# Performance work log

Measured on AMD Instinct MI355X. Metric: run time of the kernel, lower is better.

Reference implementation:

```python
import jax, jax.numpy as jnp
import numpy as np

T, IN, OUT, M, C = 8192, 1024, 1024, 128, 32
MIN_PERIOD, MAX_PERIOD = 1.0, 1024.0
LN_EPS = 1e-5


def _linear_params(key, in_f, out_f):
    # equinox nn.Linear default init: U(-1/sqrt(in), 1/sqrt(in)) for weight and bias
    lim = 1.0 / np.sqrt(in_f)
    kw, kb = jax.random.split(key)
    w = jax.random.uniform(kw, (out_f, in_f), minval=-lim, maxval=lim, dtype=jnp.float32)
    b = jax.random.uniform(kb, (out_f,), minval=-lim, maxval=lim, dtype=jnp.float32)
    return w, b


def setup_inputs() -> dict:
    key = jax.random.key(0)
    ks = jax.random.split(key, 8)
    x = jax.random.normal(ks[0], (T, IN), dtype=jnp.float32)
    done = jax.random.bernoulli(ks[1], 0.01, (T,))  # sparse episode resets
    state_re = jnp.zeros((1, M, C), jnp.float32)
    state_im = jnp.zeros((1, M, C), jnp.float32)
    # ffa.init(memory_size, context_size): decay rates a and context frequencies b
    a = jnp.linspace(1e-6, 0.5, M, dtype=jnp.float32)
    b = 2.0 * jnp.pi / jnp.linspace(MIN_PERIOD, MAX_PERIOD, C, dtype=jnp.float32)
    pre_w, pre_b = _linear_params(ks[2], IN, M)
    gin_w, gin_b = _linear_params(ks[3], IN, M)
    gout_w, gout_b = _linear_params(ks[4], IN, OUT)
    skip_w, skip_b = _linear_params(ks[5], IN, OUT)
    mix_w, mix_b = _linear_params(ks[6], 2 * M * C, OUT)
    return dict(x=x, done=done, state_re=state_re, state_im=state_im, a=a, b=b,
                pre_w=pre_w, pre_b=pre_b, gin_w=gin_w, gin_b=gin_b,
                gout_w=gout_w, gout_b=gout_b, skip_w=skip_w, skip_b=skip_b,
                mix_w=mix_w, mix_b=mix_b)


def _ffm_forward(x, done, s0, a, b, pre_w, pre_b, gin_w, gin_b,
                 gout_w, gout_b, skip_w, skip_b, mix_w, mix_b):
    # input gating: gated_x[t, m]
    gate_in = jax.nn.sigmoid(x @ gin_w.T + gin_b)            # [T, M]
    gated_x = (x @ pre_w.T + pre_b) * gate_in                # [T, M]

    # gamma[m, c] = exp(-|a_m| + i b_c): per-step complex decay/rotation
    re, im = jnp.broadcast_arrays(-jnp.abs(a)[:, None], b[None, :])
    gamma = jnp.exp(jax.lax.complex(re, im))                 # [M, C] complex64

    def step(s, inp):
        # s_t = gamma * s_{t-1} * (1 - done_t) + x_t 1^T  (reset before accumulate)
        xt, dt = inp
        keep = jnp.where(dt, 0.0, 1.0).astype(jnp.float32)
        s = keep * s * gamma + xt[:, None]
        return s, s

    _, states = jax.lax.scan(step, s0, (gated_x.astype(jnp.complex64), done))  # [T, M, C]

    # mix: concat(real, imag) along last axis -> [T, M, 2C] -> [T, 2MC]
    z_in = jnp.concatenate([states.real, states.imag], axis=-1).reshape(states.shape[0], -1)
    z = z_in @ mix_w.T + mix_b                               # [T, OUT]

    gate_out = jax.nn.sigmoid(x @ gout_w.T + gout_b)         # [T, OUT]
    skip = x @ skip_w.T + skip_b                             # [T, OUT]

    # LayerNorm without weight/bias (eps = 1e-5)
    zg = z * gate_out
    mu = zg.mean(-1, keepdims=True)
    var = ((zg - mu) ** 2).mean(-1, keepdims=True)
    ln = (zg - mu) / jnp.sqrt(var + LN_EPS)

    out = ln + skip * (1.0 - gate_out)
    return out, states


def reference(x, done, state_re, state_im, a, b, pre_w, pre_b, gin_w, gin_b,
              gout_w, gout_b, skip_w, skip_b, mix_w, mix_b):
    s0 = jax.lax.complex(state_re, state_im)[0]              # [M, C]
    return _ffm_forward(x, done, s0, a, b, pre_w, pre_b, gin_w, gin_b,
                        gout_w, gout_b, skip_w, skip_b, mix_w, mix_b)
```

## Files before the change

kernel.cpp:

```cpp
#include <hip/hip_runtime.h>
#include <stdint.h>

#define T_DIM 8192
#define IN_DIM 1024
#define OUT_DIM 1024
#define M_DIM 128
#define SEG 64
#define NSEG (T_DIM / SEG)
#define CHUNK 2048
#define KS_FB 4

typedef __bf16 bf16x8 __attribute__((ext_vector_type(8)));
typedef float f32x4 __attribute__((ext_vector_type(4)));

__device__ inline unsigned short f2bf(float f) {
  unsigned int u = __float_as_uint(f);
  unsigned int r = (u + 0x7fffu + ((u >> 16) & 1u)) >> 16;
  return (unsigned short)r;
}
__device__ inline float bf2f(unsigned short h) {
  return __uint_as_float(((unsigned int)h) << 16);
}
__device__ inline float sigm(float v) { return 1.f / (1.f + expf(-v)); }

__global__ __launch_bounds__(256) void f2bf_kernel(const float* __restrict__ in,
                                                   unsigned short* __restrict__ out, long n) {
  long i = (long)blockIdx.x * 256 + threadIdx.x;
  if (i < n) out[i] = f2bf(in[i]);
}

__global__ __launch_bounds__(256) void permconv_kernel(const float* __restrict__ w,
                                                       unsigned short* __restrict__ o, long n) {
  long i = (long)blockIdx.x * 256 + threadIdx.x;
  if (i >= n) return;
  long row = i >> 13;
  int k = (int)(i & 8191);
  int src = ((k >> 6) << 6) | ((k & 1) << 5) | ((k >> 1) & 31);
  o[i] = f2bf(w[(row << 13) + src]);
}

__global__ __launch_bounds__(256) void wcat_kernel(const float* __restrict__ gout_w,
                                                   const float* __restrict__ skip_w,
                                                   const float* __restrict__ pre_w,
                                                   const float* __restrict__ gin_w,
                                                   unsigned short* __restrict__ o) {
  long i = (long)blockIdx.x * 256 + threadIdx.x;
  if (i >= (long)2304 * 1024) return;
  int row = (int)(i >> 10), col = (int)(i & 1023);
  float v;
  if (row < 1024)       v = gout_w[row * 1024 + col];
  else if (row < 2048)  v = skip_w[(row - 1024) * 1024 + col];
  else if (row < 2176)  v = pre_w[(row - 2048) * 1024 + col];
  else                  v = gin_w[(row - 2176) * 1024 + col];
  o[i] = f2bf(v);
}

__global__ void bcat_kernel(const float* __restrict__ gout_b, const float* __restrict__ skip_b,
                            const float* __restrict__ pre_b, const float* __restrict__ gin_b,
                            float* __restrict__ dst) {
  int i = blockIdx.x * 256 + threadIdx.x;
  if (i >= 2304) return;
  float v;
  if (i < 1024)      v = gout_b[i];
  else if (i < 2048) v = skip_b[i - 1024];
  else if (i < 2176) v = pre_b[i - 2048];
  else               v = gin_b[i - 2176];
  dst[i] = v;
}

__global__ void gamma_kernel(const float* __restrict__ a, const float* __restrict__ b,
                             float2* __restrict__ gam, float2* __restrict__ gamL) {
  int tid = blockIdx.x * 256 + threadIdx.x;
  int m = tid >> 5, c = tid & 31;
  double aa = fabs((double)a[m]);
  double ang = (double)b[c];
  double mag = exp(-aa);
  gam[tid] = make_float2((float)(mag * cos(ang)), (float)(mag * sin(ang)));
  double magL = exp(-aa * (double)SEG);
  double angL = ang * (double)SEG;
  gamL[tid] = make_float2((float)(magL * cos(angL)), (float)(magL * sin(angL)));
}

#define GEMM_KLOOP(AP, BP, LDK)                                                        \
  for (int k0 = 0; k0 < kloop_end; k0 += 64) {                                         \
    _Pragma("unroll")                                                                  \
    for (int cc = 0; cc < 4; ++cc) {                                                   \
      __builtin_amdgcn_global_load_lds(                                                \
          (const __attribute__((address_space(1))) void*)(AP + k0 + (size_t)cc * 32 * (LDK)), \
          (__attribute__((address_space(3))) void*)(As + cc * 2048 + w * 512), 16, 0, 0);     \
      __builtin_amdgcn_global_load_lds(                                                \
          (const __attribute__((address_space(1))) void*)(BP + k0 + (size_t)cc * 32 * (LDK)), \
          (__attribute__((address_space(3))) void*)(Bs + cc * 2048 + w * 512), 16, 0, 0);     \
    }                                                                                  \
    __syncthreads();                                                                   \
    _Pragma("unroll")                                                                  \
    for (int kk = 0; kk < 2; ++kk) {                                                   \
      const int eb = kk ? e1 : e0;                                                     \
      const char* Bp = (const char*)Bpbase + eb;                                       \
      bf16x8 b0 = *(const bf16x8*)(Bp);                                                \
      bf16x8 b1 = *(const bf16x8*)(Bp + 2048);                                         \
      bf16x8 b2 = *(const bf16x8*)(Bp + 4096);                                         \
      bf16x8 b3 = *(const bf16x8*)(Bp + 6144);                                         \
      const char* Ap = (const char*)Apbase + eb;                                       \
      _Pragma("unroll")                                                                \
      for (int i = 0; i < 4; ++i) {                                                    \
        bf16x8 af = *(const bf16x8*)(Ap + i * 2048);                                   \
        acc[i][0] = __builtin_amdgcn_mfma_f32_16x16x32_bf16(af, b0, acc[i][0], 0, 0, 0);\
        acc[i][1] = __builtin_amdgcn_mfma_f32_16x16x32_bf16(af, b1, acc[i][1], 0, 0, 0);\
        acc[i][2] = __builtin_amdgcn_mfma_f32_16x16x32_bf16(af, b2, acc[i][2], 0, 0, 0);\
        acc[i][3] = __builtin_amdgcn_mfma_f32_16x16x32_bf16(af, b3, acc[i][3], 0, 0, 0);\
      }                                                                                \
    }                                                                                  \
    __syncthreads();                                                                   \
  }

#define GEMM_PREAMBLE                                                                  \
  const int tid = threadIdx.x;                                                         \
  const int lane = tid & 63, w = tid >> 6;                                             \
  const int wr = w >> 1, wc = w & 1;                                                   \
  f32x4 acc[4][4] = {};                                                                \
  const int srow = tid >> 3;                                                           \
  const int ksw = ((tid & 7) ^ (srow & 7)) * 8;                                        \
  const int l15 = lane & 15;                                                           \
  const int krd = (lane >> 4) * 8;                                                     \
  const int rsw = (lane & 7) << 3;                                                     \
  const int e0 = (krd ^ rsw) * 2;                                                      \
  const int e1 = ((32 + krd) ^ rsw) * 2;                                               \
  const unsigned short* Apbase = &As[(wr * 64 + l15) * 64];                            \
  const unsigned short* Bpbase = &Bs[(wc * 64 + l15) * 64];

__global__ __launch_bounds__(256, 4) void gemm_gs_kernel(
    const unsigned short* __restrict__ A, const unsigned short* __restrict__ B,
    const float* __restrict__ bias, unsigned short* __restrict__ gs,
    float* __restrict__ tmp) {
  __shared__ __align__(16) unsigned short As[128 * 64];
  __shared__ __align__(16) unsigned short Bs[128 * 64];
  const int xcd = blockIdx.x & 7;
  const int idx = blockIdx.x >> 3;
  const int bn = idx % 18;
  const int bm = xcd * 8 + idx / 18;
  const int n0 = bn * 128, t0 = bm * 128;
  GEMM_PREAMBLE
  const unsigned short* Ab = A + (size_t)(t0 + srow) * 1024 + ksw;
  const unsigned short* Bb = B + (size_t)(n0 + srow) * 1024 + ksw;
  const int kloop_end = 1024;
  GEMM_KLOOP(Ab, Bb, 1024)

  const int rbase = t0 + wr * 64 + ((lane >> 4) * 4);
  const int cbase = n0 + wc * 64 + l15;
#pragma unroll
  for (int j = 0; j < 4; ++j) {
    const int col = cbase + j * 16;
    const float bv = bias[col];
#pragma unroll
    for (int i = 0; i < 4; ++i) {
#pragma unroll
      for (int r = 0; r < 4; ++r) {
        float v = acc[i][j][r] + bv;
        int row = rbase + i * 16 + r;
        if (col < 2048) gs[(size_t)row * 2048 + col] = f2bf(v);
        else            tmp[(size_t)row * 256 + (col - 2048)] = v;
      }
    }
  }
}

__global__ __launch_bounds__(256, 4) void gemm_splitk_kernel(
    const unsigned short* __restrict__ A, const unsigned short* __restrict__ B,
    float* __restrict__ partials, int nbm, int kslice, int prows, int xcd_map) {
  __shared__ __align__(16) unsigned short As[128 * 64];
  __shared__ __align__(16) unsigned short Bs[128 * 64];
  int bm, bn, ks;
  if (xcd_map) {
    const int xcd = blockIdx.x & 7;
    const int idx = blockIdx.x >> 3;
    ks = xcd >> 2;
    bm = (xcd & 3) * 16 + (idx >> 3);
    bn = idx & 7;
  } else {
    const int cpx = gridDim.x >> 3;
    const int wid = (blockIdx.x & 7) * cpx + (blockIdx.x >> 3);
    bm = wid % nbm;
    bn = (wid / nbm) & 7;
    ks = wid / (nbm * 8);
  }
  const int n0 = bn * 128, t0 = bm * 128;
  GEMM_PREAMBLE
  const unsigned short* Ab = A + (size_t)(t0 + srow) * 8192 + ks * kslice + ksw;
  const unsigned short* Bb = B + (size_t)(n0 + srow) * 8192 + ks * kslice + ksw;
  const int kloop_end = kslice;
  GEMM_KLOOP(Ab, Bb, 8192)

  float* Cp = partials + (size_t)ks * prows * 1024;
  const int rbase = t0 + wr * 64 + ((lane >> 4) * 4);
  const int cbase = n0 + wc * 64 + l15;
#pragma unroll
  for (int j = 0; j < 4; ++j) {
    const int col = cbase + j * 16;
#pragma unroll
    for (int i = 0; i < 4; ++i)
#pragma unroll
      for (int r = 0; r < 4; ++r)
        Cp[(size_t)(rbase + i * 16 + r) * 1024 + col] = acc[i][j][r];
  }
}

__global__ __launch_bounds__(256) void reduce_kernel(const f32x4* __restrict__ partials,
                                                     const f32x4* __restrict__ bias4,
                                                     f32x4* __restrict__ outc) {
  int i = blockIdx.x * 256 + threadIdx.x;
  const size_t stride = (size_t)CHUNK * 256;
  f32x4 s = partials[i];
#pragma unroll
  for (int p = 1; p < KS_FB; ++p) s += partials[(size_t)p * stride + i];
  s += bias4[i & 255];
  outc[i] = s;
}

__global__ __launch_bounds__(256) void gated_kernel(const float* __restrict__ tmp,
                                                    float* __restrict__ gated) {
  int i = blockIdx.x * 256 + threadIdx.x;
  int t = i >> 7, m = i & 127;
  float p = tmp[t * 256 + m];
  float g = tmp[t * 256 + 128 + m];
  gated[i] = p * sigm(g);
}

__global__ __launch_bounds__(256) void scan_p1_kernel(
    const float* __restrict__ gated, const int* __restrict__ done,
    const float2* __restrict__ gam, const float2* __restrict__ gamL,
    float2* __restrict__ carryA, float2* __restrict__ carryB) {
  int gid = blockIdx.x * 256 + threadIdx.x;
  int seg = gid >> 12, tid = gid & 4095;
  int m = tid >> 5;
  float2 g = gam[tid];
  int t0 = seg * SEG;
  float sr = 0.f, si = 0.f, keep_all = 1.f;
  for (int tt = 0; tt < SEG; ++tt) {
    int t = t0 + tt;
    float xv = gated[t * M_DIM + m];
    bool d = done[t] != 0;
    float pr = d ? 0.f : sr;
    float pi = d ? 0.f : si;
    if (d) keep_all = 0.f;
    sr = fmaf(g.x, pr, fmaf(-g.y, pi, xv));
    si = fmaf(g.y, pr, g.x * pi);
  }
  carryB[(size_t)seg * 4096 + tid] = make_float2(sr, si);
  float2 gL = gamL[tid];
  carryA[(size_t)seg * 4096 + tid] = make_float2(keep_all * gL.x, keep_all * gL.y);
}

__global__ __launch_bounds__(256) void scan_p2_kernel(
    const float2* __restrict__ carryA, float2* __restrict__ carryB,
    const float* __restrict__ s0_re, const float* __restrict__ s0_im) {
  int tid = blockIdx.x * 256 + threadIdx.x;
  float sr = s0_re[tid], si = s0_im[tid];
  for (int p = 0; p < NSEG; ++p) {
    size_t idx = (size_t)p * 4096 + tid;
    float2 A = carryA[idx];
    float2 B = carryB[idx];
    carryB[idx] = make_float2(sr, si);
    float nr = fmaf(A.x, sr, fmaf(-A.y, si, B.x));
    float ni = fmaf(A.y, sr, fmaf(A.x, si, B.y));
    sr = nr; si = ni;
  }
}

__global__ __launch_bounds__(256) void scan_p3_kernel(
    const float* __restrict__ gated, const int* __restrict__ done,
    const float2* __restrict__ gam, const float2* __restrict__ segstart,
    float* __restrict__ out_states, int pair_mode,
    unsigned int* __restrict__ st_bf, int tbase) {
  int gid = blockIdx.x * 256 + threadIdx.x;
  int segl = gid >> 12, tid = gid & 4095;
  int m = tid >> 5;
  int seg = tbase / SEG + segl;
  float2 g = gam[tid];
  float2 s = segstart[(size_t)seg * 4096 + tid];
  float sr = s.x, si = s.y;
  int t0 = seg * SEG;
  for (int tt = 0; tt < SEG; ++tt) {
    int t = t0 + tt;
    float xv = gated[t * M_DIM + m];
    bool d = done[t] != 0;
    float pr = d ? 0.f : sr;
    float pi = d ? 0.f : si;
    sr = fmaf(g.x, pr, fmaf(-g.y, pi, xv));
    si = fmaf(g.y, pr, g.x * pi);
    if (pair_mode) {
      ((float2*)out_states)[(size_t)t * 4096 + tid] = make_float2(sr, si);
    } else {
      out_states[(size_t)t * 4096 + tid] = sr;
    }
    st_bf[(size_t)(t - tbase) * 4096 + tid] =
        (unsigned int)f2bf(sr) | ((unsigned int)f2bf(si) << 16);
  }
}

__global__ __launch_bounds__(256) void ln_kernel(const float* __restrict__ partials, int nred,
                                                 const float* __restrict__ mixb,
                                                 const unsigned short* __restrict__ gs,
                                                 float* __restrict__ out) {
  const int t = blockIdx.x;
  const int tid = threadIdx.x;
  __shared__ float sm[8];
  const int o = tid * 4;
  f32x4 z;
  if (nred == 0) {
    z = *(const f32x4*)&out[(size_t)t * 1024 + o];
  } else {
    z = *(const f32x4*)&partials[(size_t)t * 1024 + o];
    for (int p = 1; p < nred; ++p)
      z += *(const f32x4*)&partials[(size_t)p * T_DIM * 1024 + (size_t)t * 1024 + o];
    z += *(const f32x4*)&mixb[o];
  }
  ushort4 gu = *(const ushort4*)&gs[(size_t)t * 2048 + o];
  ushort4 su = *(const ushort4*)&gs[(size_t)t * 2048 + 1024 + o];
  float g[4], sk[4], zg[4];
  g[0] = sigm(bf2f(gu.x)); g[1] = sigm(bf2f(gu.y));
  g[2] = sigm(bf2f(gu.z)); g[3] = sigm(bf2f(gu.w));
  sk[0] = bf2f(su.x); sk[1] = bf2f(su.y); sk[2] = bf2f(su.z); sk[3] = bf2f(su.w);
  float sum = 0.f;
#pragma unroll
  for (int j = 0; j < 4; ++j) { zg[j] = z[j] * g[j]; sum += zg[j]; }
#pragma unroll
  for (int off = 32; off > 0; off >>= 1) sum += __shfl_down(sum, off, 64);
  if ((tid & 63) == 0) sm[tid >> 6] = sum;
  __syncthreads();
  const float mu = (sm[0] + sm[1] + sm[2] + sm[3]) * (1.f / 1024.f);
  float sq = 0.f;
#pragma unroll
  for (int j = 0; j < 4; ++j) { float d = zg[j] - mu; sq += d * d; }
#pragma unroll
  for (int off = 32; off > 0; off >>= 1) sq += __shfl_down(sq, off, 64);
  if ((tid & 63) == 0) sm[4 + (tid >> 6)] = sq;
  __syncthreads();
  const float var = (sm[4] + sm[5] + sm[6] + sm[7]) * (1.f / 1024.f);
  const float rstd = 1.f / sqrtf(var + 1e-5f);
  f32x4 res;
#pragma unroll
  for (int j = 0; j < 4; ++j) res[j] = (zg[j] - mu) * rstd + sk[j] * (1.f - g[j]);
  *(f32x4*)&out[(size_t)t * 1024 + o] = res;
}

extern "C" void kernel_launch(void* const* d_in, const int* in_sizes, int n_in,
                              void* d_out, int out_size, void* d_ws, size_t ws_size,
                              hipStream_t stream) {
  const float* x      = (const float*)d_in[0];
  const int*   done   = (const int*)d_in[1];
  const float* s0_re  = (const float*)d_in[2];
  const float* s0_im  = (const float*)d_in[3];
  const float* a      = (const float*)d_in[4];
  const float* b      = (const float*)d_in[5];
  const float* pre_w  = (const float*)d_in[6];
  const float* pre_b  = (const float*)d_in[7];
  const float* gin_w  = (const float*)d_in[8];
  const float* gin_b  = (const float*)d_in[9];
  const float* gout_w = (const float*)d_in[10];
  const float* gout_b = (const float*)d_in[11];
  const float* skip_w = (const float*)d_in[12];
  const float* skip_b = (const float*)d_in[13];
  const float* mix_w  = (const float*)d_in[14];
  const float* mix_b  = (const float*)d_in[15];

  float* out_f = (float*)d_out;
  float* states_f = out_f + (size_t)T_DIM * OUT_DIM;
  const int pair_mode = (out_size >= 75000000) ? 1 : 0;

  char* ws = (char*)d_ws;
  size_t off = 0;
  auto alloc = [&](size_t bytes) {
    void* p = ws + off;
    off = (off + bytes + 255) & ~(size_t)255;
    return p;
  };
  unsigned short* x_bf   = (unsigned short*)alloc((size_t)T_DIM * IN_DIM * 2);
  unsigned short* Bmix   = (unsigned short*)alloc((size_t)OUT_DIM * 8192 * 2);
  unsigned short* Wgs    = (unsigned short*)alloc((size_t)2304 * IN_DIM * 2);
  float* bias_gs         = (float*)alloc(2304 * 4);
  float* tmp_pg          = (float*)alloc((size_t)T_DIM * 256 * 4);
  float* gated           = (float*)alloc((size_t)T_DIM * M_DIM * 4);
  float2* gam            = (float2*)alloc(4096 * 8);
  float2* gamL           = (float2*)alloc(4096 * 8);
  float2* carryA         = (float2*)alloc((size_t)NSEG * 4096 * 8);
  float2* carryB         = (float2*)alloc((size_t)NSEG * 4096 * 8);
  unsigned short* gs_o   = (unsigned short*)alloc((size_t)T_DIM * 2048 * 2);

  size_t need_main = off + (size_t)T_DIM * 8192 * 2 + (size_t)2 * T_DIM * 1024 * 4 + 1024;
  const int full_path = (ws_size == 0 || ws_size >= need_main) ? 1 : 0;

  dim3 blk(256);
  long nx = (long)T_DIM * IN_DIM;
  f2bf_kernel<<<(unsigned)((nx + 255) / 256), blk, 0, stream>>>(x, x_bf, nx);
  permconv_kernel<<<32768, blk, 0, stream>>>(mix_w, Bmix, 8388608L);
  wcat_kernel<<<9216, blk, 0, stream>>>(gout_w, skip_w, pre_w, gin_w, Wgs);
  bcat_kernel<<<9, blk, 0, stream>>>(gout_b, skip_b, pre_b, gin_b, bias_gs);
  gamma_kernel<<<16, blk, 0, stream>>>(a, b, gam, gamL);

  gemm_gs_kernel<<<1152, blk, 0, stream>>>(x_bf, Wgs, bias_gs, gs_o, tmp_pg);
  gated_kernel<<<(T_DIM * M_DIM) / 256, blk, 0, stream>>>(tmp_pg, gated);

  scan_p1_kernel<<<NSEG * 16, blk, 0, stream>>>(gated, done, gam, gamL, carryA, carryB);
  scan_p2_kernel<<<16, blk, 0, stream>>>(carryA, carryB, s0_re, s0_im);

  if (full_path) {
    unsigned short* st_bf = (unsigned short*)alloc((size_t)T_DIM * 8192 * 2);
    float* partials       = (float*)alloc((size_t)2 * T_DIM * 1024 * 4);
    scan_p3_kernel<<<NSEG * 16, blk, 0, stream>>>(gated, done, gam, carryB,
                                                  states_f, pair_mode,
                                                  (unsigned int*)st_bf, 0);
    gemm_splitk_kernel<<<1024, blk, 0, stream>>>(st_bf, Bmix, partials,
                                                 64, 4096, T_DIM, 1);
    ln_kernel<<<T_DIM, blk, 0, stream>>>(partials, 2, mix_b, gs_o, out_f);
  } else {
    unsigned short* st_bf = (unsigned short*)alloc((size_t)CHUNK * 8192 * 2);
    float* partials       = (float*)alloc((size_t)KS_FB * CHUNK * 1024 * 4);
    for (int ch = 0; ch < T_DIM / CHUNK; ++ch) {
      int tbase = ch * CHUNK;
      scan_p3_kernel<<<(CHUNK / SEG) * 16, blk, 0, stream>>>(gated, done, gam, carryB,
                                                             states_f, pair_mode,
                                                             (unsigned int*)st_bf, tbase);
      gemm_splitk_kernel<<<8 * (CHUNK / 128) * KS_FB, blk, 0, stream>>>(
          st_bf, Bmix, partials, CHUNK / 128, 8192 / KS_FB, CHUNK, 0);
      reduce_kernel<<<CHUNK, blk, 0, stream>>>((const f32x4*)partials, (const f32x4*)mix_b,
                                               (f32x4*)(out_f + (size_t)tbase * OUT_DIM));
    }
    ln_kernel<<<T_DIM, blk, 0, stream>>>(nullptr, 0, mix_b, gs_o, out_f);
  }
  (void)n_in; (void)in_sizes;
}
```

Before: 370.4 us.

## Use 256x256-tile double-buffered GEMM for the mix projection

```diff
diff --git a/kernel.cpp b/kernel.cpp
--- a/kernel.cpp
+++ b/kernel.cpp
@@ -165,25 +165,113 @@
   }
 }
 
+__global__ __launch_bounds__(512, 2) void gemm_mix256_kernel(
+    const unsigned short* __restrict__ A, const unsigned short* __restrict__ B,
+    float* __restrict__ partials) {
+  __shared__ __align__(16) unsigned short As[2][256 * 64];
+  __shared__ __align__(16) unsigned short Bs[2][256 * 64];
+  const int xcd = blockIdx.x & 7;
+  const int idx = blockIdx.x >> 3;
+  const int ks = xcd >> 2;
+  const int bm = (xcd & 3) * 8 + (idx >> 2);
+  const int bn = idx & 3;
+  const int t0 = bm * 256, n0 = bn * 256;
+  const int tid = threadIdx.x;
+  const int lane = tid & 63;
+  const int w8 = tid >> 6;
+  const int wr = w8 >> 2;
+  const int wcol = w8 & 3;
+
+  f32x4 acc[8][4] = {};
+
+  const int srow = tid >> 3;
+  const int ksw = ((tid & 7) ^ (srow & 7)) * 8;
+  const unsigned short* Ab = A + (size_t)(t0 + srow) * 8192 + ks * 4096 + ksw;
+  const unsigned short* Bb = B + (size_t)(n0 + srow) * 8192 + ks * 4096 + ksw;
+
+  const int l15 = lane & 15;
+  const int krd = (lane >> 4) * 8;
+  const int rsw = (lane & 7) << 3;
+  const int e0 = (krd ^ rsw) * 2;
+  const int e1 = ((32 + krd) ^ rsw) * 2;
+
+#define STAGE256(buf, k0c)                                                              \
+  {                                                                                     \
+    _Pragma("unroll")                                                                   \
+    for (int j = 0; j < 4; ++j)                                                         \
+      __builtin_amdgcn_global_load_lds(                                                 \
+          (const __attribute__((address_space(1))) void*)(Ab + (k0c) + (size_t)j * 64 * 8192), \
+          (__attribute__((address_space(3))) void*)(&As[buf][j * 4096 + tid * 8]), 16, 0, 0);  \
+    _Pragma("unroll")                                                                   \
+    for (int j = 0; j < 4; ++j)                                                         \
+      __builtin_amdgcn_global_load_lds(                                                 \
+          (const __attribute__((address_space(1))) void*)(Bb + (k0c) + (size_t)j * 64 * 8192), \
+          (__attribute__((address_space(3))) void*)(&Bs[buf][j * 4096 + tid * 8]), 16, 0, 0);  \
+  }
+
+  const int iters = 4096 / 64;
+  STAGE256(0, 0)
+  int cur = 0;
+
+  for (int t = 0; t < iters; ++t) {
+    __builtin_amdgcn_s_barrier();
+    __builtin_amdgcn_sched_barrier(0);
+    const int k1 = (t + 1 < iters) ? (t + 1) * 64 : t * 64;
+    if (cur) { STAGE256(0, k1) } else { STAGE256(1, k1) }
+    __builtin_amdgcn_sched_barrier(0);
+    asm volatile("s_waitcnt vmcnt(8)" ::: "memory");
+    __builtin_amdgcn_sched_barrier(0);
+    __builtin_amdgcn_s_barrier();
+    __builtin_amdgcn_sched_barrier(0);
+
+    const unsigned short* Apb = &As[cur][(wr * 128 + l15) * 64];
+    const unsigned short* Bpb = &Bs[cur][(wcol * 64 + l15) * 64];
+#pragma unroll
+    for (int s = 0; s < 2; ++s) {
+      const int eb = s ? e1 : e0;
+      bf16x8 bf0 = *(const bf16x8*)((const char*)Bpb + eb);
+      bf16x8 bf1 = *(const bf16x8*)((const char*)Bpb + 2048 + eb);
+      bf16x8 bf2 = *(const bf16x8*)((const char*)Bpb + 4096 + eb);
+      bf16x8 bf3 = *(const bf16x8*)((const char*)Bpb + 6144 + eb);
+      __builtin_amdgcn_s_setprio(1);
+#pragma unroll
+      for (int i = 0; i < 8; ++i) {
+        bf16x8 af = *(const bf16x8*)((const char*)Apb + i * 2048 + eb);
+        acc[i][0] = __builtin_amdgcn_mfma_f32_16x16x32_bf16(af, bf0, acc[i][0], 0, 0, 0);
+        acc[i][1] = __builtin_amdgcn_mfma_f32_16x16x32_bf16(af, bf1, acc[i][1], 0, 0, 0);
+        acc[i][2] = __builtin_amdgcn_mfma_f32_16x16x32_bf16(af, bf2, acc[i][2], 0, 0, 0);
+        acc[i][3] = __builtin_amdgcn_mfma_f32_16x16x32_bf16(af, bf3, acc[i][3], 0, 0, 0);
+      }
+      __builtin_amdgcn_s_setprio(0);
+    }
+    cur ^= 1;
+  }
+
+  float* Cp = partials + (size_t)ks * T_DIM * 1024;
+  const int rbase = t0 + wr * 128 + ((lane >> 4) * 4);
+  const int cbase = n0 + wcol * 64 + l15;
+#pragma unroll
+  for (int j = 0; j < 4; ++j) {
+    const int col = cbase + j * 16;
+#pragma unroll
+    for (int i = 0; i < 8; ++i)
+#pragma unroll
+      for (int r = 0; r < 4; ++r)
+        Cp[(size_t)(rbase + i * 16 + r) * 1024 + col] = acc[i][j][r];
+  }
+#undef STAGE256
+}
+
 __global__ __launch_bounds__(256, 4) void gemm_splitk_kernel(
     const unsigned short* __restrict__ A, const unsigned short* __restrict__ B,
-    float* __restrict__ partials, int nbm, int kslice, int prows, int xcd_map) {
+    float* __restrict__ partials, int nbm, int kslice, int prows) {
   __shared__ __align__(16) unsigned short As[128 * 64];
   __shared__ __align__(16) unsigned short Bs[128 * 64];
-  int bm, bn, ks;
-  if (xcd_map) {
-    const int xcd = blockIdx.x & 7;
-    const int idx = blockIdx.x >> 3;
-    ks = xcd >> 2;
-    bm = (xcd & 3) * 16 + (idx >> 3);
-    bn = idx & 7;
-  } else {
-    const int cpx = gridDim.x >> 3;
-    const int wid = (blockIdx.x & 7) * cpx + (blockIdx.x >> 3);
-    bm = wid % nbm;
-    bn = (wid / nbm) & 7;
-    ks = wid / (nbm * 8);
-  }
+  const int cpx = gridDim.x >> 3;
+  const int wid = (blockIdx.x & 7) * cpx + (blockIdx.x >> 3);
+  const int bm = wid % nbm;
+  const int bn = (wid / nbm) & 7;
+  const int ks = wid / (nbm * 8);
   const int n0 = bn * 128, t0 = bm * 128;
   GEMM_PREAMBLE
   const unsigned short* Ab = A + (size_t)(t0 + srow) * 8192 + ks * kslice + ksw;
@@ -410,8 +498,7 @@
     scan_p3_kernel<<<NSEG * 16, blk, 0, stream>>>(gated, done, gam, carryB,
                                                   states_f, pair_mode,
                                                   (unsigned int*)st_bf, 0);
-    gemm_splitk_kernel<<<1024, blk, 0, stream>>>(st_bf, Bmix, partials,
-                                                 64, 4096, T_DIM, 1);
+    gemm_mix256_kernel<<<256, dim3(512), 0, stream>>>(st_bf, Bmix, partials);
     ln_kernel<<<T_DIM, blk, 0, stream>>>(partials, 2, mix_b, gs_o, out_f);
   } else {
     unsigned short* st_bf = (unsigned short*)alloc((size_t)CHUNK * 8192 * 2);
@@ -422,7 +509,7 @@
                                                              states_f, pair_mode,
                                                              (unsigned int*)st_bf, tbase);
       gemm_splitk_kernel<<<8 * (CHUNK / 128) * KS_FB, blk, 0, stream>>>(
-          st_bf, Bmix, partials, CHUNK / 128, 8192 / KS_FB, CHUNK, 0);
+          st_bf, Bmix, partials, CHUNK / 128, 8192 / KS_FB, CHUNK);
       reduce_kernel<<<CHUNK, blk, 0, stream>>>((const f32x4*)partials, (const f32x4*)mix_b,
                                                (f32x4*)(out_f + (size_t)tbase * OUT_DIM));
     }
```

Result: no change. 371.4 us (+0.3%).
